# Kernel optimization log

Measured on AMD Instinct MI355X. Metric: run time of the kernel, lower is better.

The kernel has to match this reference:

```python
import jax, jax.numpy as jnp
import numpy as np

B, T, HID = 2, 2048, 2048
NH, NKV, HD = 16, 4, 128
GROUPS = NH // NKV

def _rotate_half(t):
    t1, t2 = jnp.split(t, 2, axis=-1)
    return jnp.concatenate([-t2, t1], axis=-1)

def _apply_rotary(t, cos, sin):
    # t: [B, H, T, D], cos/sin: [1, 1, T, D]
    return t * cos + _rotate_half(t) * sin

def setup_inputs() -> dict:
    key = jax.random.key(0)
    ks = jax.random.split(key, 6)
    x = jax.random.normal(ks[0], (B, T, HID), dtype=jnp.float32)
    # real rotary tables
    inv_freq = 1.0 / (10000.0 ** (jnp.arange(0, HD, 2, dtype=jnp.float32) / HD))
    pos = jnp.arange(T, dtype=jnp.float32)
    freqs = jnp.outer(pos, inv_freq)            # [T, D/2]
    emb = jnp.concatenate([freqs, freqs], -1)   # [T, D]
    cos = jnp.cos(emb)[None, None]              # [1,1,T,D]
    sin = jnp.sin(emb)[None, None]
    s = 0.02
    Wq = jax.random.normal(ks[1], (HID, NH * HD), dtype=jnp.float32) * s
    Wk = jax.random.normal(ks[2], (HID, NKV * HD), dtype=jnp.float32) * s
    Wv = jax.random.normal(ks[3], (HID, NKV * HD), dtype=jnp.float32) * s
    Wo = jax.random.normal(ks[4], (NH * HD, HID), dtype=jnp.float32) * s
    return {"x": x, "cos": cos, "sin": sin, "Wq": Wq, "Wk": Wk, "Wv": Wv, "Wo": Wo}

def reference(x, cos, sin, Wq, Wk, Wv, Wo):
    b, t, _ = x.shape
    q = (x @ Wq).reshape(b, t, NH, HD).transpose(0, 2, 1, 3)    # [B,NH,T,D]
    k = (x @ Wk).reshape(b, t, NKV, HD).transpose(0, 2, 1, 3)   # [B,NKV,T,D]
    v = (x @ Wv).reshape(b, t, NKV, HD).transpose(0, 2, 1, 3)
    q = _apply_rotary(q, cos, sin)
    k = _apply_rotary(k, cos, sin)
    # GQA without repeat_interleave: group q-heads by kv-head
    qg = q.reshape(b, NKV, GROUPS, t, HD)                       # [B,KV,G,T,D]
    scale = 1.0 / jnp.sqrt(jnp.float32(HD))
    scores = jnp.einsum('bkgtd,bksd->bkgts', qg, k) * scale     # [B,KV,G,T,S]
    causal = jnp.tril(jnp.ones((t, t), dtype=bool))
    scores = jnp.where(causal[None, None, None], scores, jnp.float32(-1e30))
    attn = jax.nn.softmax(scores, axis=-1)
    out = jnp.einsum('bkgts,bksd->bkgtd', attn, v)              # [B,KV,G,T,D]
    out = out.reshape(b, NH, t, HD).transpose(0, 2, 1, 3).reshape(b, t, NH * HD)
    return out @ Wo
```

## Files before the change

kernel.cpp:

```cpp
#include <hip/hip_runtime.h>
#include <hip/hip_bf16.h>
#include <cstdint>

typedef unsigned short u16;
typedef unsigned int u32;
typedef __bf16 bf16x8 __attribute__((ext_vector_type(8)));
typedef float f32x4 __attribute__((ext_vector_type(4)));

#define BDIM 2
#define TDIM 2048
#define HIDDIM 2048
#define NHEAD 16
#define NKVH 4
#define HD 128
#define MROWS (BDIM*TDIM)
#define NQKV 3072
#define KDIM 2048

#define MFMA16(a,b,c) __builtin_amdgcn_mfma_f32_16x16x32_bf16((a),(b),(c),0,0,0)

__device__ __forceinline__ u16 f2bf(float f) {
    __bf16 h = (__bf16)f;
    return __builtin_bit_cast(u16, h);
}
__device__ __forceinline__ float bf2f(u32 u) {
    u <<= 16;
    return __builtin_bit_cast(float, u);
}
__device__ __forceinline__ void gld16(const void* g, void* l) {
    __builtin_amdgcn_global_load_lds(
        (const __attribute__((address_space(1))) u32*)g,
        (__attribute__((address_space(3))) u32*)l, 16, 0, 0);
}

__global__ __launch_bounds__(256) void cvt_x_kernel(const float* __restrict__ x,
                                                    u16* __restrict__ o) {
    size_t i = ((size_t)blockIdx.x * 256 + threadIdx.x) * 8;
    float4 a = *(const float4*)(x + i);
    float4 b = *(const float4*)(x + i + 4);
    uint4 v;
    v.x = (u32)f2bf(a.x) | ((u32)f2bf(a.y) << 16);
    v.y = (u32)f2bf(a.z) | ((u32)f2bf(a.w) << 16);
    v.z = (u32)f2bf(b.x) | ((u32)f2bf(b.y) << 16);
    v.w = (u32)f2bf(b.z) | ((u32)f2bf(b.w) << 16);
    *(uint4*)(o + i) = v;
}

__global__ __launch_bounds__(256) void transpose_cvt(const float* __restrict__ src,
                                                     u16* __restrict__ dst, int N) {
    __shared__ float tile[32][33];
    int tx = threadIdx.x, ty = threadIdx.y;
    int n0 = blockIdx.x * 32, k0 = blockIdx.y * 32;
#pragma unroll
    for (int r = 0; r < 4; r++)
        tile[ty + 8*r][tx] = src[(size_t)(k0 + ty + 8*r) * N + n0 + tx];
    __syncthreads();
#pragma unroll
    for (int r = 0; r < 4; r++)
        dst[(size_t)(n0 + ty + 8*r) * KDIM + k0 + tx] = f2bf(tile[tx][ty + 8*r]);
}

template<int OUT_BF16>
__global__ void __launch_bounds__(256, 2) gemm_bt(const u16* __restrict__ A,
                                                  const u16* __restrict__ Bt,
                                                  void* __restrict__ C, int ldc) {
    __shared__ __align__(16) u16 Al[128 * 32];
    __shared__ __align__(16) u16 Bl[128 * 32];
    const int tid = threadIdx.x;
    const int lane = tid & 63;
    const int w = tid >> 6;
    const int wm = (w & 1) * 64;
    const int wn = (w >> 1) * 64;
    const int quad = lane >> 4;
    const int l15 = lane & 15;
    const size_t bm = (size_t)blockIdx.x * 128;
    const size_t bn = (size_t)blockIdx.y * 128;

    const int srow = lane >> 2;
    const int kq = (lane & 3) ^ ((lane >> 3) & 3);
    const int i0 = 2 * w, i1 = 2 * w + 1;

    const u16* ga0 = A + (bm + i0*16 + srow) * KDIM + kq * 8;
    const u16* ga1 = A + (bm + i1*16 + srow) * KDIM + kq * 8;
    const u16* gb0 = Bt + (bn + i0*16 + srow) * KDIM + kq * 8;
    const u16* gb1 = Bt + (bn + i1*16 + srow) * KDIM + kq * 8;

    const int swz = ((quad ^ ((l15 >> 1) & 3)) << 3);
    int aoff[4], boff[4];
#pragma unroll
    for (int t = 0; t < 4; t++) {
        aoff[t] = (wm + t*16 + l15) * 32 + swz;
        boff[t] = (wn + t*16 + l15) * 32 + swz;
    }

    f32x4 acc[4][4] = {};

    for (int kt = 0; kt < KDIM / 32; kt++) {
        gld16(ga0 + kt*32, &Al[i0 * 512]);
        gld16(ga1 + kt*32, &Al[i1 * 512]);
        gld16(gb0 + kt*32, &Bl[i0 * 512]);
        gld16(gb1 + kt*32, &Bl[i1 * 512]);
        __syncthreads();
        bf16x8 af[4], bfv[4];
#pragma unroll
        for (int t = 0; t < 4; t++) {
            af[t]  = *(const bf16x8*)&Al[aoff[t]];
            bfv[t] = *(const bf16x8*)&Bl[boff[t]];
        }
#pragma unroll
        for (int mt = 0; mt < 4; mt++)
#pragma unroll
            for (int nt = 0; nt < 4; nt++)
                acc[mt][nt] = MFMA16(af[mt], bfv[nt], acc[mt][nt]);
        __syncthreads();
    }

#pragma unroll
    for (int mt = 0; mt < 4; mt++) {
        size_t m0 = bm + wm + mt*16 + quad*4;
#pragma unroll
        for (int nt = 0; nt < 4; nt++) {
            size_t n = bn + wn + nt*16 + l15;
#pragma unroll
            for (int r = 0; r < 4; r++) {
                if (OUT_BF16)
                    ((u16*)C)[(m0 + r) * (size_t)ldc + n] = f2bf(acc[mt][nt][r]);
                else
                    ((float*)C)[(m0 + r) * (size_t)ldc + n] = acc[mt][nt][r];
            }
        }
    }
}

__global__ __launch_bounds__(256) void rotary_kernel(u16* __restrict__ QKV,
                                                     const float* __restrict__ cosT,
                                                     const float* __restrict__ sinT) {
    int i = blockIdx.x * 256 + threadIdx.x;
    int m = i / 320;
    int rem = i - m * 320;
    int head = rem >> 4;
    int d0 = (rem & 15) << 2;
    int t = m & (TDIM - 1);
    int col;
    float sc;
    if (head < NHEAD) {
        col = head * HD + d0;
        sc = 0.08838834764831845f * 1.4426950408889634f;
    } else {
        col = HIDDIM + (head - NHEAD) * HD + d0;
        sc = 1.0f;
    }
    u16* p0 = QKV + (size_t)m * NQKV + col;
    u16* p1 = p0 + 64;
    float4 cv = *(const float4*)(cosT + t * HD + d0);
    float4 sv = *(const float4*)(sinT + t * HD + d0);
    uint2 qa = *(const uint2*)p0;
    uint2 qb = *(const uint2*)p1;
    float f0[4] = { bf2f(qa.x & 0xffffu), bf2f(qa.x >> 16), bf2f(qa.y & 0xffffu), bf2f(qa.y >> 16) };
    float f1[4] = { bf2f(qb.x & 0xffffu), bf2f(qb.x >> 16), bf2f(qb.y & 0xffffu), bf2f(qb.y >> 16) };
    float c[4] = { cv.x, cv.y, cv.z, cv.w };
    float s[4] = { sv.x, sv.y, sv.z, sv.w };
    u16 o0[4], o1[4];
#pragma unroll
    for (int k = 0; k < 4; k++) {
        o0[k] = f2bf((f0[k] * c[k] - f1[k] * s[k]) * sc);
        o1[k] = f2bf((f1[k] * c[k] + f0[k] * s[k]) * sc);
    }
    uint2 w0, w1;
    w0.x = (u32)o0[0] | ((u32)o0[1] << 16);
    w0.y = (u32)o0[2] | ((u32)o0[3] << 16);
    w1.x = (u32)o1[0] | ((u32)o1[1] << 16);
    w1.y = (u32)o1[2] | ((u32)o1[3] << 16);
    *(uint2*)p0 = w0;
    *(uint2*)p1 = w1;
}

__global__ void __launch_bounds__(256, 2) attn_kernel(const u16* __restrict__ QKV,
                                                      u16* __restrict__ AO) {
    constexpr int LV = 72;
    constexpr int LP = 72;
    __shared__ __align__(16) u16 Kl[64 * 128];
    __shared__ __align__(16) u16 Vt[128 * LV];

    const int pa = blockIdx.x;
    const int h  = blockIdx.y;
    const int b  = blockIdx.z;
    const int kh = h >> 2;
    const int tid = threadIdx.x;
    const int lane = tid & 63;
    const int w = tid >> 6;
    const int quad = lane >> 4;
    const int l15 = lane & 15;

    const size_t rowbase = (size_t)b * TDIM;
    const u16* Qb = QKV + rowbase * NQKV + h * HD;
    const u16* Kb = QKV + rowbase * NQKV + HIDDIM + kh * HD;
    const u16* Vb = Kb + NKVH * HD;

    int krow[4], kgch[4];
#pragma unroll
    for (int i = 0; i < 4; i++) {
        krow[i] = w*16 + i*4 + quad;
        kgch[i] = l15 ^ (krow[i] & 7);
    }

#pragma unroll 1
    for (int ph = 0; ph < 2; ph++) {
        const int qt = ph ? (31 - pa) : pa;

        bf16x8 qf[4];
        {
            const u16* qr = Qb + (size_t)(qt*64 + w*16 + l15) * NQKV;
#pragma unroll
            for (int kt = 0; kt < 4; kt++)
                qf[kt] = *(const bf16x8*)(qr + kt*32 + quad*8);
        }
        f32x4 O[8] = {};
        float mrun[4], lrun[4];
#pragma unroll
        for (int r = 0; r < 4; r++) { mrun[r] = -1e30f; lrun[r] = 0.0f; }

#pragma unroll 1
        for (int j = 0; j <= qt; j++) {
#pragma unroll
            for (int i = 0; i < 4; i++) {
                const u16* g = Kb + (size_t)(j*64 + krow[i]) * NQKV + kgch[i]*8;
                gld16(g, &Kl[(w*16 + i*4) * 128]);
            }
#pragma unroll
            for (int i = 0; i < 2; i++) {
                int u = tid + 256*i;
                int sp = u & 31, dch = u >> 5;
                int s = sp*2, d0 = dch*8;
                const u16* g0 = Vb + (size_t)(j*64 + s) * NQKV + d0;
                uint4 r0 = *(const uint4*)g0;
                uint4 r1 = *(const uint4*)(g0 + NQKV);
                u32 ra[4] = { r0.x, r0.y, r0.z, r0.w };
                u32 rb[4] = { r1.x, r1.y, r1.z, r1.w };
#pragma unroll
                for (int k2 = 0; k2 < 4; k2++) {
                    u32 lo = (ra[k2] & 0xffffu) | (rb[k2] << 16);
                    u32 hi = (ra[k2] >> 16) | (rb[k2] & 0xffff0000u);
                    *(u32*)&Vt[(d0 + 2*k2)     * LV + s] = lo;
                    *(u32*)&Vt[(d0 + 2*k2 + 1) * LV + s] = hi;
                }
            }
            __syncthreads();

            f32x4 S[4] = {};
#pragma unroll
            for (int kt = 0; kt < 4; kt++) {
                int p = (kt*4 + quad) ^ (l15 & 7);
#pragma unroll
                for (int nt = 0; nt < 4; nt++) {
                    bf16x8 bfr = *(const bf16x8*)&Kl[(nt*16 + l15)*128 + p*8];
                    S[nt] = MFMA16(qf[kt], bfr, S[nt]);
                }
            }

            if (j == qt) {
                int toff = w*16 + quad*4;
#pragma unroll
                for (int nt = 0; nt < 4; nt++) {
                    int scol = nt*16 + l15;
#pragma unroll
                    for (int r = 0; r < 4; r++)
                        if (scol > toff + r) S[nt][r] = -1e30f;
                }
            }

            float alpha[4];
#pragma unroll
            for (int r = 0; r < 4; r++) {
                float mx = fmaxf(fmaxf(S[0][r], S[1][r]), fmaxf(S[2][r], S[3][r]));
                mx = fmaxf(mx, __shfl_xor(mx, 1));
                mx = fmaxf(mx, __shfl_xor(mx, 2));
                mx = fmaxf(mx, __shfl_xor(mx, 4));
                mx = fmaxf(mx, __shfl_xor(mx, 8));
                float mnew = fmaxf(mrun[r], mx);
                float al = __builtin_amdgcn_exp2f(mrun[r] - mnew);
                mrun[r] = mnew;
                alpha[r] = al;
                float rs = 0.0f;
#pragma unroll
                for (int nt = 0; nt < 4; nt++) {
                    float p = __builtin_amdgcn_exp2f(S[nt][r] - mnew);
                    S[nt][r] = p;
                    rs += p;
                }
                rs += __shfl_xor(rs, 1);
                rs += __shfl_xor(rs, 2);
                rs += __shfl_xor(rs, 4);
                rs += __shfl_xor(rs, 8);
                lrun[r] = lrun[r] * al + rs;
            }
#pragma unroll
            for (int nt = 0; nt < 8; nt++)
#pragma unroll
                for (int r = 0; r < 4; r++)
                    O[nt][r] *= alpha[r];

            __syncthreads();
#pragma unroll
            for (int nt = 0; nt < 4; nt++)
#pragma unroll
                for (int r = 0; r < 4; r++)
                    Kl[(w*16 + quad*4 + r) * LP + nt*16 + l15] = f2bf(S[nt][r]);
            __syncthreads();

#pragma unroll
            for (int kt = 0; kt < 2; kt++) {
                bf16x8 pa_f = *(const bf16x8*)&Kl[(w*16 + l15) * LP + kt*32 + quad*8];
#pragma unroll
                for (int nt = 0; nt < 8; nt++) {
                    bf16x8 bv = *(const bf16x8*)&Vt[(nt*16 + l15) * LV + kt*32 + quad*8];
                    O[nt] = MFMA16(pa_f, bv, O[nt]);
                }
            }
            __syncthreads();
        }

        float inv[4];
#pragma unroll
        for (int r = 0; r < 4; r++) inv[r] = 1.0f / lrun[r];
        size_t row0 = rowbase + qt*64 + w*16 + quad*4;
#pragma unroll
        for (int nt = 0; nt < 8; nt++) {
            size_t cix = (size_t)h * HD + nt*16 + l15;
#pragma unroll
            for (int r = 0; r < 4; r++)
                AO[(row0 + r) * HIDDIM + cix] = f2bf(O[nt][r] * inv[r]);
        }
    }
}

extern "C" void kernel_launch(void* const* d_in, const int* in_sizes, int n_in,
                              void* d_out, int out_size, void* d_ws, size_t ws_size,
                              hipStream_t stream) {
    (void)in_sizes; (void)n_in; (void)out_size; (void)ws_size;
    const float* x    = (const float*)d_in[0];
    const float* cosT = (const float*)d_in[1];
    const float* sinT = (const float*)d_in[2];
    const float* Wq   = (const float*)d_in[3];
    const float* Wk   = (const float*)d_in[4];
    const float* Wv   = (const float*)d_in[5];
    const float* Wo   = (const float*)d_in[6];

    char* ws = (char*)d_ws;
    u16* QKV   = (u16*)ws;
    u16* xb    = (u16*)(ws + (size_t)MROWS * NQKV * 2);
    u16* Wqkvt = (u16*)(ws + (size_t)MROWS * NQKV * 2 + (size_t)MROWS * HIDDIM * 2);
    u16* Wot   = Wqkvt + (size_t)NQKV * KDIM;

    cvt_x_kernel<<<4096, 256, 0, stream>>>(x, xb);
    dim3 tb(32, 8);
    transpose_cvt<<<dim3(64, 64), tb, 0, stream>>>(Wq, Wqkvt, 2048);
    transpose_cvt<<<dim3(16, 64), tb, 0, stream>>>(Wk, Wqkvt + (size_t)2048 * KDIM, 512);
    transpose_cvt<<<dim3(16, 64), tb, 0, stream>>>(Wv, Wqkvt + (size_t)2560 * KDIM, 512);
    transpose_cvt<<<dim3(64, 64), tb, 0, stream>>>(Wo, Wot, 2048);

    gemm_bt<1><<<dim3(32, 24), 256, 0, stream>>>(xb, Wqkvt, QKV, NQKV);
    rotary_kernel<<<5120, 256, 0, stream>>>(QKV, cosT, sinT);
    attn_kernel<<<dim3(16, 16, 2), 256, 0, stream>>>(QKV, xb);
    gemm_bt<0><<<dim3(32, 16), 256, 0, stream>>>(xb, Wot, d_out, HIDDIM);
}
```

Before: 334.8 us.

## Double-buffer K tiles and register-prefetch V in attention loop

Prefetches the next K tile into a second LDS buffer with async loads and holds the next V tile in registers while the current tile is computed, so global loads overlap with MFMA work. P moves to its own LDS buffer, which removes two barriers per iteration. V transpose storage switches from padded rows to an XOR-swizzled layout, and the O rescale is skipped when no row max changed. LDS use grows, which may lower occupancy at the requested 2 blocks per CU.

```diff
diff --git a/kernel.cpp b/kernel.cpp
--- a/kernel.cpp
+++ b/kernel.cpp
@@ -177,10 +177,10 @@
 
 __global__ void __launch_bounds__(256, 2) attn_kernel(const u16* __restrict__ QKV,
                                                       u16* __restrict__ AO) {
-    constexpr int LV = 72;
     constexpr int LP = 72;
-    __shared__ __align__(16) u16 Kl[64 * 128];
-    __shared__ __align__(16) u16 Vt[128 * LV];
+    __shared__ __align__(16) u16 Kl[2][64 * 128];
+    __shared__ __align__(16) u16 Vt[128 * 64];
+    __shared__ __align__(16) u16 Pl[64 * LP];
 
     const int pa = blockIdx.x;
     const int h  = blockIdx.y;
@@ -203,6 +203,9 @@
         krow[i] = w*16 + i*4 + quad;
         kgch[i] = l15 ^ (krow[i] & 7);
     }
+    const int sp0 = tid & 31, dch0 = tid >> 5;
+    const int sp1 = sp0, dch1 = dch0 + 8;
+    const int vq0 = quad ^ (l15 >> 3);
 
 #pragma unroll 1
     for (int ph = 0; ph < 2; ph++) {
@@ -220,40 +223,70 @@
 #pragma unroll
         for (int r = 0; r < 4; r++) { mrun[r] = -1e30f; lrun[r] = 0.0f; }
 
+#pragma unroll
+        for (int i = 0; i < 4; i++)
+            gld16(Kb + (size_t)krow[i] * NQKV + kgch[i]*8, &Kl[0][(w*16 + i*4) * 128]);
+        uint4 vr0a, vr0b, vr1a, vr1b;
+        {
+            const u16* g0 = Vb + (size_t)(sp0*2) * NQKV + dch0*8;
+            vr0a = *(const uint4*)g0;
+            vr0b = *(const uint4*)(g0 + NQKV);
+            const u16* g1 = Vb + (size_t)(sp1*2) * NQKV + dch1*8;
+            vr1a = *(const uint4*)g1;
+            vr1b = *(const uint4*)(g1 + NQKV);
+        }
+
 #pragma unroll 1
         for (int j = 0; j <= qt; j++) {
-#pragma unroll
-            for (int i = 0; i < 4; i++) {
-                const u16* g = Kb + (size_t)(j*64 + krow[i]) * NQKV + kgch[i]*8;
-                gld16(g, &Kl[(w*16 + i*4) * 128]);
-            }
-#pragma unroll
-            for (int i = 0; i < 2; i++) {
-                int u = tid + 256*i;
-                int sp = u & 31, dch = u >> 5;
-                int s = sp*2, d0 = dch*8;
-                const u16* g0 = Vb + (size_t)(j*64 + s) * NQKV + d0;
-                uint4 r0 = *(const uint4*)g0;
-                uint4 r1 = *(const uint4*)(g0 + NQKV);
-                u32 ra[4] = { r0.x, r0.y, r0.z, r0.w };
-                u32 rb[4] = { r1.x, r1.y, r1.z, r1.w };
+            {
+                u32 ra[4] = { vr0a.x, vr0a.y, vr0a.z, vr0a.w };
+                u32 rb[4] = { vr0b.x, vr0b.y, vr0b.z, vr0b.w };
+                int sx = (sp0*2) ^ ((dch0 & 3) << 3);
+                int d0 = dch0 * 8;
 #pragma unroll
                 for (int k2 = 0; k2 < 4; k2++) {
                     u32 lo = (ra[k2] & 0xffffu) | (rb[k2] << 16);
                     u32 hi = (ra[k2] >> 16) | (rb[k2] & 0xffff0000u);
-                    *(u32*)&Vt[(d0 + 2*k2)     * LV + s] = lo;
-                    *(u32*)&Vt[(d0 + 2*k2 + 1) * LV + s] = hi;
+                    *(u32*)&Vt[(d0 + 2*k2)     * 64 + sx] = lo;
+                    *(u32*)&Vt[(d0 + 2*k2 + 1) * 64 + sx] = hi;
+                }
+                u32 rc[4] = { vr1a.x, vr1a.y, vr1a.z, vr1a.w };
+                u32 rd[4] = { vr1b.x, vr1b.y, vr1b.z, vr1b.w };
+                sx = (sp1*2) ^ ((dch1 & 3) << 3);
+                d0 = dch1 * 8;
+#pragma unroll
+                for (int k2 = 0; k2 < 4; k2++) {
+                    u32 lo = (rc[k2] & 0xffffu) | (rd[k2] << 16);
+                    u32 hi = (rc[k2] >> 16) | (rd[k2] & 0xffff0000u);
+                    *(u32*)&Vt[(d0 + 2*k2)     * 64 + sx] = lo;
+                    *(u32*)&Vt[(d0 + 2*k2 + 1) * 64 + sx] = hi;
                 }
             }
             __syncthreads();
 
+            if (j < qt) {
+                const u16* Kbn = Kb + (size_t)(j+1) * 64 * NQKV;
+                u16* kl = Kl[(j+1) & 1];
+#pragma unroll
+                for (int i = 0; i < 4; i++)
+                    gld16(Kbn + (size_t)krow[i] * NQKV + kgch[i]*8, &kl[(w*16 + i*4) * 128]);
+                const u16* Vbn = Vb + (size_t)(j+1) * 64 * NQKV;
+                const u16* g0 = Vbn + (size_t)(sp0*2) * NQKV + dch0*8;
+                vr0a = *(const uint4*)g0;
+                vr0b = *(const uint4*)(g0 + NQKV);
+                const u16* g1 = Vbn + (size_t)(sp1*2) * NQKV + dch1*8;
+                vr1a = *(const uint4*)g1;
+                vr1b = *(const uint4*)(g1 + NQKV);
+            }
+
+            const u16* kl = Kl[j & 1];
             f32x4 S[4] = {};
 #pragma unroll
             for (int kt = 0; kt < 4; kt++) {
                 int p = (kt*4 + quad) ^ (l15 & 7);
 #pragma unroll
                 for (int nt = 0; nt < 4; nt++) {
-                    bf16x8 bfr = *(const bf16x8*)&Kl[(nt*16 + l15)*128 + p*8];
+                    bf16x8 bfr = *(const bf16x8*)&kl[(nt*16 + l15)*128 + p*8];
                     S[nt] = MFMA16(qf[kt], bfr, S[nt]);
                 }
             }
@@ -294,26 +327,29 @@
                 rs += __shfl_xor(rs, 8);
                 lrun[r] = lrun[r] * al + rs;
             }
-#pragma unroll
-            for (int nt = 0; nt < 8; nt++)
+            bool need = (alpha[0] < 1.0f) | (alpha[1] < 1.0f) |
+                        (alpha[2] < 1.0f) | (alpha[3] < 1.0f);
+            if (__any(need)) {
+#pragma unroll
+                for (int nt = 0; nt < 8; nt++)
+#pragma unroll
+                    for (int r = 0; r < 4; r++)
+                        O[nt][r] *= alpha[r];
+            }
+
+#pragma unroll
+            for (int nt = 0; nt < 4; nt++)
 #pragma unroll
                 for (int r = 0; r < 4; r++)
-                    O[nt][r] *= alpha[r];
-
-            __syncthreads();
-#pragma unroll
-            for (int nt = 0; nt < 4; nt++)
-#pragma unroll
-                for (int r = 0; r < 4; r++)
-                    Kl[(w*16 + quad*4 + r) * LP + nt*16 + l15] = f2bf(S[nt][r]);
-            __syncthreads();
+                    Pl[(w*16 + quad*4 + r) * LP + nt*16 + l15] = f2bf(S[nt][r]);
 
 #pragma unroll
             for (int kt = 0; kt < 2; kt++) {
-                bf16x8 pa_f = *(const bf16x8*)&Kl[(w*16 + l15) * LP + kt*32 + quad*8];
+                bf16x8 pa_f = *(const bf16x8*)&Pl[(w*16 + l15) * LP + kt*32 + quad*8];
 #pragma unroll
                 for (int nt = 0; nt < 8; nt++) {
-                    bf16x8 bv = *(const bf16x8*)&Vt[(nt*16 + l15) * LV + kt*32 + quad*8];
+                    int qp = vq0 ^ ((nt & 1) << 1);
+                    bf16x8 bv = *(const bf16x8*)&Vt[(nt*16 + l15) * 64 + kt*32 + qp*8];
                     O[nt] = MFMA16(pa_f, bv, O[nt]);
                 }
             }
```

New measurement: 343.3 us. 1.03x slower.
